# Performance work log

Hardware: AMD Instinct MI355X
Metric: run time of the kernel (lower is better)

The kernel has to match this reference:

```python
import jax, jax.numpy as jnp
import numpy as np

N_NODES = 100000
N_EDGES = 1600000
D = 128


def _gine_layer(x, src, dst, e, W1, b1, W2, b2):
    # message: relu(x_j + e_ji), aggregate: sum at destination
    m = jax.nn.relu(x[src] + e)                       # [E, D]
    agg = jax.ops.segment_sum(m, dst, num_segments=x.shape[0])  # [N, D]
    h = agg + x                                       # (1 + eps) * x_i with eps = 0
    h = jax.nn.relu(jnp.dot(h, W1) + b1)
    return jnp.dot(h, W2) + b2


def setup_inputs() -> dict:
    key = jax.random.key(0)
    ks = jax.random.split(key, 16)
    s = 0.05
    inp = {
        "x": jax.random.normal(ks[0], (N_NODES, D), dtype=jnp.float32),
        "edge_index": jax.random.randint(ks[1], (2, N_EDGES), 0, N_NODES, dtype=jnp.int64) if jax.config.jax_enable_x64 else jax.random.randint(ks[1], (2, N_EDGES), 0, N_NODES, dtype=jnp.int32),
        "edge_attr": jax.random.randint(ks[2], (N_EDGES,), 0, 100, dtype=jnp.int32),
        "edge_emb": jax.random.normal(ks[3], (100, D), dtype=jnp.float32) * s,
        "Win": jax.random.normal(ks[4], (D, D), dtype=jnp.float32) * s,
        "b_in": jnp.zeros((D,), dtype=jnp.float32),
        "W1_0": jax.random.normal(ks[5], (D, D), dtype=jnp.float32) * s,
        "b1_0": jnp.zeros((D,), dtype=jnp.float32),
        "W2_0": jax.random.normal(ks[6], (D, D), dtype=jnp.float32) * s,
        "b2_0": jnp.zeros((D,), dtype=jnp.float32),
        "W1_1": jax.random.normal(ks[7], (D, D), dtype=jnp.float32) * s,
        "b1_1": jnp.zeros((D,), dtype=jnp.float32),
        "W2_1": jax.random.normal(ks[8], (D, D), dtype=jnp.float32) * s,
        "b2_1": jnp.zeros((D,), dtype=jnp.float32),
        "Wout": jax.random.normal(ks[9], (D, 1), dtype=jnp.float32) * s,
        "b_out": jnp.zeros((1,), dtype=jnp.float32),
    }
    return inp


def reference(x, edge_index, edge_attr, edge_emb, Win, b_in,
              W1_0, b1_0, W2_0, b2_0, W1_1, b1_1, W2_1, b2_1,
              Wout, b_out):
    src, dst = edge_index[0], edge_index[1]
    e = edge_emb[edge_attr]                 # [E, D] edge-attribute embedding lookup
    h = jnp.dot(x, Win) + b_in              # input_proj
    # layer 0: GINEConv + residual add + relu (norm=none, dropout off)
    h = jax.nn.relu(_gine_layer(h, src, dst, e, W1_0, b1_0, W2_0, b2_0) + h)
    # layer 1
    h = jax.nn.relu(_gine_layer(h, src, dst, e, W1_1, b1_1, W2_1, b2_1) + h)
    # output_mlp: single Linear(hidden, 1); no final activation, no pooling
    return jnp.dot(h, Wout) + b_out
```

## Files before the change

### kernel.cpp

```cpp
#include <hip/hip_runtime.h>

#define NN 100000
#define D 128
#define CHUNK 4096
#define BCSTRIDE 392
#define AGG_BLOCKS 1024

typedef __attribute__((ext_vector_type(8))) short short8;
typedef __attribute__((ext_vector_type(8))) unsigned short ushort8;
typedef __attribute__((ext_vector_type(4))) float f32x4;

__device__ __forceinline__ float4 ld4(const float* p) { return *(const float4*)p; }

__device__ __forceinline__ unsigned short f2bf(float f) {
    unsigned int u = __float_as_uint(f);
    unsigned int r = u + 0x7fffu + ((u >> 16) & 1u);
    return (unsigned short)(r >> 16);
}
__device__ __forceinline__ float bf2f(unsigned short h) {
    return __uint_as_float(((unsigned int)h) << 16);
}
__device__ __forceinline__ int swz(int r, int c) {
    return r * 128 + ((((c >> 2) ^ (r & 7)) << 2) | (c & 3));
}

__device__ __forceinline__ void coop_gemm(
    const unsigned int* uT,
    const unsigned short* __restrict__ Whi, const unsigned short* __restrict__ Wlo,
    int wv, int L, int lr, int q, f32x4 acc[4][2])
{
    #pragma unroll
    for (int ks = 0; ks < 4; ++ks) {
        short8 ahi[4], alo[4];
        #pragma unroll
        for (int m = 0; m < 4; ++m) {
            const int row = m * 16 + lr;
            const int cb  = ks * 32 + q * 8;
            const uint4 a0 = *(const uint4*)&uT[swz(row, cb)];
            const uint4 a1 = *(const uint4*)&uT[swz(row, cb + 4)];
            const unsigned int w[8] = {a0.x, a0.y, a0.z, a0.w, a1.x, a1.y, a1.z, a1.w};
            #pragma unroll
            for (int j = 0; j < 8; ++j) {
                ahi[m][j] = (short)(w[j] >> 16);
                alo[m][j] = (short)(w[j] & 0xffffu);
            }
        }
        #pragma unroll
        for (int n = 0; n < 2; ++n) {
            const int nt = wv * 2 + n;
            const int base = ((nt * 4 + ks) * 64 + L) * 8;
            const short8 bhi = *(const short8*)&Whi[base];
            const short8 blo = *(const short8*)&Wlo[base];
            #pragma unroll
            for (int m = 0; m < 4; ++m) {
                acc[m][n] = __builtin_amdgcn_mfma_f32_16x16x32_bf16(alo[m], bhi, acc[m][n], 0, 0, 0);
                acc[m][n] = __builtin_amdgcn_mfma_f32_16x16x32_bf16(ahi[m], blo, acc[m][n], 0, 0, 0);
                acc[m][n] = __builtin_amdgcn_mfma_f32_16x16x32_bf16(ahi[m], bhi, acc[m][n], 0, 0, 0);
            }
        }
    }
}

__global__ __launch_bounds__(256) void setup_all(
    const float* __restrict__ W0, const float* __restrict__ W1,
    const float* __restrict__ W2, const float* __restrict__ W3,
    const float* __restrict__ W4, unsigned short* __restrict__ wp,
    const float* __restrict__ emb, unsigned int* __restrict__ embp,
    int* __restrict__ binTotal)
{
    const int T = blockIdx.x * 256 + threadIdx.x;
    if (T < 5 * D * D) {
        const int w = T / (D * D);
        const int t = T % (D * D);
        const float* W = (w == 0) ? W0 : (w == 1) ? W1 : (w == 2) ? W2 : (w == 3) ? W3 : W4;
        const int j  = t & 7;
        const int L  = (t >> 3) & 63;
        const int ks = (t >> 9) & 3;
        const int nt = t >> 11;
        const float v = W[(ks * 32 + (L >> 4) * 8 + j) * D + nt * 16 + (L & 15)];
        const unsigned short h = f2bf(v);
        unsigned short* hi = wp + (size_t)w * 2 * D * D;
        hi[t] = h;
        hi[D * D + t] = f2bf(v - bf2f(h));
    } else if (T < 5 * D * D + 6400) {
        const int i = T - 5 * D * D;
        embp[i] = (unsigned int)f2bf(emb[i * 2]) | ((unsigned int)f2bf(emb[i * 2 + 1]) << 16);
    } else if (T < 5 * D * D + 6400 + BCSTRIDE) {
        binTotal[T - 5 * D * D - 6400] = 0;
    }
}

__global__ __launch_bounds__(256) void gemm_in(
    const float* __restrict__ A1,
    const unsigned short* __restrict__ Whi, const unsigned short* __restrict__ Wlo,
    const float* __restrict__ bias,
    unsigned short* __restrict__ out_hi, unsigned short* __restrict__ out_lo, int N)
{
    __shared__ __align__(16) unsigned int uT[64 * 128];
    const int t  = threadIdx.x;
    const int wv = t >> 6;
    const int L  = t & 63;
    const int lr = L & 15;
    const int q  = L >> 4;
    const int rbase = wv * 16;
    const int row = blockIdx.x * 64 + rbase + lr;
    const int rl  = rbase + lr;

    #pragma unroll
    for (int ks = 0; ks < 4; ++ks) {
        float v[8];
        if (row < N) {
            const int off = row * D + ks * 32 + q * 8;
            const float4 x0 = ld4(&A1[off]), x1 = ld4(&A1[off + 4]);
            v[0] = x0.x; v[1] = x0.y; v[2] = x0.z; v[3] = x0.w;
            v[4] = x1.x; v[5] = x1.y; v[6] = x1.z; v[7] = x1.w;
        } else {
            #pragma unroll
            for (int j = 0; j < 8; ++j) v[j] = 0.f;
        }
        unsigned int pk[8];
        #pragma unroll
        for (int j = 0; j < 8; ++j) {
            const unsigned int hi = f2bf(v[j]);
            pk[j] = (hi << 16) | f2bf(v[j] - bf2f((unsigned short)hi));
        }
        const int cb = ks * 32 + q * 8;
        *(uint4*)&uT[swz(rl, cb)]     = make_uint4(pk[0], pk[1], pk[2], pk[3]);
        *(uint4*)&uT[swz(rl, cb + 4)] = make_uint4(pk[4], pk[5], pk[6], pk[7]);
    }
    __syncthreads();

    f32x4 acc[4][2];
    #pragma unroll
    for (int m = 0; m < 4; ++m)
        #pragma unroll
        for (int n = 0; n < 2; ++n) acc[m][n] = (f32x4){0.f, 0.f, 0.f, 0.f};
    coop_gemm(uT, Whi, Wlo, wv, L, lr, q, acc);
    __syncthreads();

    #pragma unroll
    for (int n = 0; n < 2; ++n) {
        const int nt = wv * 2 + n;
        const float b = bias[nt * 16 + lr];
        #pragma unroll
        for (int m = 0; m < 4; ++m)
            #pragma unroll
            for (int r = 0; r < 4; ++r)
                uT[swz(m * 16 + q * 4 + r, nt * 16 + lr)] = __float_as_uint(acc[m][n][r] + b);
    }
    __syncthreads();

    if (row < N) {
        #pragma unroll
        for (int ks = 0; ks < 4; ++ks) {
            const int cb = ks * 32 + q * 8;
            const uint4 a0 = *(const uint4*)&uT[swz(rl, cb)];
            const uint4 a1 = *(const uint4*)&uT[swz(rl, cb + 4)];
            const unsigned int w[8] = {a0.x, a0.y, a0.z, a0.w, a1.x, a1.y, a1.z, a1.w};
            const int off = row * D + cb;
            ushort8 oh, ol;
            #pragma unroll
            for (int j = 0; j < 8; ++j) {
                const float o = __uint_as_float(w[j]);
                const unsigned short h = f2bf(o);
                oh[j] = h;
                ol[j] = f2bf(o - bf2f(h));
            }
            *(ushort8*)&out_hi[off] = oh;
            *(ushort8*)&out_lo[off] = ol;
        }
    }
}

template<bool LAST>
__global__ __launch_bounds__(256) void mlp_fused(
    const float* __restrict__ agg,
    const unsigned short* h_hi, const unsigned short* h_lo,
    const unsigned short* __restrict__ W1hi, const unsigned short* __restrict__ W1lo,
    const float* __restrict__ b1,
    const unsigned short* __restrict__ W2hi, const unsigned short* __restrict__ W2lo,
    const float* __restrict__ b2,
    unsigned short* out_hi, unsigned short* out_lo,
    const float* __restrict__ Wout, const float* __restrict__ bout,
    float* __restrict__ outv, int N)
{
    __shared__ __align__(16) unsigned int uT[64 * 128];
    const int t  = threadIdx.x;
    const int wv = t >> 6;
    const int L  = t & 63;
    const int lr = L & 15;
    const int q  = L >> 4;
    const int rbase = wv * 16;
    const int row = blockIdx.x * 64 + rbase + lr;
    const int rl  = rbase + lr;

    #pragma unroll
    for (int ks = 0; ks < 4; ++ks) {
        float v[8];
        if (row < N) {
            const int off = row * D + ks * 32 + q * 8;
            const float4 x0 = ld4(&agg[off]), x1 = ld4(&agg[off + 4]);
            const ushort8 hh = *(const ushort8*)&h_hi[off];
            const ushort8 ll = *(const ushort8*)&h_lo[off];
            v[0] = x0.x; v[1] = x0.y; v[2] = x0.z; v[3] = x0.w;
            v[4] = x1.x; v[5] = x1.y; v[6] = x1.z; v[7] = x1.w;
            #pragma unroll
            for (int j = 0; j < 8; ++j) v[j] += bf2f(hh[j]) + bf2f(ll[j]);
        } else {
            #pragma unroll
            for (int j = 0; j < 8; ++j) v[j] = 0.f;
        }
        unsigned int pk[8];
        #pragma unroll
        for (int j = 0; j < 8; ++j) {
            const unsigned int hi = f2bf(v[j]);
            pk[j] = (hi << 16) | f2bf(v[j] - bf2f((unsigned short)hi));
        }
        const int cb = ks * 32 + q * 8;
        *(uint4*)&uT[swz(rl, cb)]     = make_uint4(pk[0], pk[1], pk[2], pk[3]);
        *(uint4*)&uT[swz(rl, cb + 4)] = make_uint4(pk[4], pk[5], pk[6], pk[7]);
    }
    __syncthreads();

    f32x4 acc[4][2];
    #pragma unroll
    for (int m = 0; m < 4; ++m)
        #pragma unroll
        for (int n = 0; n < 2; ++n) acc[m][n] = (f32x4){0.f, 0.f, 0.f, 0.f};
    coop_gemm(uT, W1hi, W1lo, wv, L, lr, q, acc);
    __syncthreads();

    #pragma unroll
    for (int n = 0; n < 2; ++n) {
        const int nt = wv * 2 + n;
        const float b = b1[nt * 16 + lr];
        #pragma unroll
        for (int m = 0; m < 4; ++m)
            #pragma unroll
            for (int r = 0; r < 4; ++r) {
                const float o = fmaxf(acc[m][n][r] + b, 0.f);
                const unsigned int hi = f2bf(o);
                const unsigned int lo = f2bf(o - bf2f((unsigned short)hi));
                uT[swz(m * 16 + q * 4 + r, nt * 16 + lr)] = (hi << 16) | lo;
            }
    }
    __syncthreads();

    f32x4 acc2[4][2];
    #pragma unroll
    for (int m = 0; m < 4; ++m)
        #pragma unroll
        for (int n = 0; n < 2; ++n) acc2[m][n] = (f32x4){0.f, 0.f, 0.f, 0.f};
    coop_gemm(uT, W2hi, W2lo, wv, L, lr, q, acc2);
    __syncthreads();

    #pragma unroll
    for (int n = 0; n < 2; ++n) {
        const int nt = wv * 2 + n;
        const float b = b2[nt * 16 + lr];
        #pragma unroll
        for (int m = 0; m < 4; ++m)
            #pragma unroll
            for (int r = 0; r < 4; ++r)
                uT[swz(m * 16 + q * 4 + r, nt * 16 + lr)] = __float_as_uint(acc2[m][n][r] + b);
    }
    __syncthreads();

    if (LAST) {
        float accv = 0.f;
        if (row < N) {
            #pragma unroll
            for (int ks = 0; ks < 4; ++ks) {
                const int cb = ks * 32 + q * 8;
                const uint4 a0 = *(const uint4*)&uT[swz(rl, cb)];
                const uint4 a1 = *(const uint4*)&uT[swz(rl, cb + 4)];
                const unsigned int w[8] = {a0.x, a0.y, a0.z, a0.w, a1.x, a1.y, a1.z, a1.w};
                const int off = row * D + cb;
                const ushort8 hh = *(const ushort8*)&h_hi[off];
                const ushort8 ll = *(const ushort8*)&h_lo[off];
                const float4 w0 = ld4(&Wout[cb]);
                const float4 w1 = ld4(&Wout[cb + 4]);
                float o[8];
                #pragma unroll
                for (int j = 0; j < 8; ++j)
                    o[j] = fmaxf(__uint_as_float(w[j]) + bf2f(hh[j]) + bf2f(ll[j]), 0.f);
                accv += o[0] * w0.x + o[1] * w0.y + o[2] * w0.z + o[3] * w0.w;
                accv += o[4] * w1.x + o[5] * w1.y + o[6] * w1.z + o[7] * w1.w;
            }
        }
        accv += __shfl_xor(accv, 16);
        accv += __shfl_xor(accv, 32);
        if (q == 0 && row < N) outv[row] = accv + bout[0];
    } else if (row < N) {
        #pragma unroll
        for (int ks = 0; ks < 4; ++ks) {
            const int cb = ks * 32 + q * 8;
            const uint4 a0 = *(const uint4*)&uT[swz(rl, cb)];
            const uint4 a1 = *(const uint4*)&uT[swz(rl, cb + 4)];
            const unsigned int w[8] = {a0.x, a0.y, a0.z, a0.w, a1.x, a1.y, a1.z, a1.w};
            const int off = row * D + cb;
            const ushort8 hh = *(const ushort8*)&h_hi[off];
            const ushort8 ll = *(const ushort8*)&h_lo[off];
            ushort8 oh, ol;
            #pragma unroll
            for (int j = 0; j < 8; ++j) {
                const float o = fmaxf(__uint_as_float(w[j]) + bf2f(hh[j]) + bf2f(ll[j]), 0.f);
                const unsigned short h = f2bf(o);
                oh[j] = h;
                ol[j] = f2bf(o - bf2f(h));
            }
            *(ushort8*)&out_hi[off] = oh;
            *(ushort8*)&out_lo[off] = ol;
        }
    }
}

__global__ __launch_bounds__(256) void bin_count(
    const int* __restrict__ dst, int* __restrict__ blkcnt,
    int* __restrict__ binTotal, int E, int nbins)
{
    __shared__ int hist[512];
    const int t = threadIdx.x;
    const int i = blockIdx.x;
    for (int k = t; k < nbins; k += 256) hist[k] = 0;
    __syncthreads();
    const int e0 = i * CHUNK;
    const int e1 = min(E, e0 + CHUNK);
    for (int e = e0 + t; e < e1; e += 256) atomicAdd(&hist[dst[e] >> 8], 1);
    __syncthreads();
    for (int k = t; k < nbins; k += 256) {
        const int c = hist[k];
        blkcnt[i * BCSTRIDE + k] = c;
        if (c) atomicAdd(&binTotal[k], c);
    }
}

__global__ __launch_bounds__(512) void bin_scan(
    const int* __restrict__ binTotal, int* __restrict__ binStart,
    int* __restrict__ binCursor, int nbins)
{
    __shared__ int s[512];
    const int t = threadIdx.x;
    const int v = (t < nbins) ? binTotal[t] : 0;
    s[t] = v;
    __syncthreads();
    for (int off = 1; off < 512; off <<= 1) {
        const int x = (t >= off) ? s[t - off] : 0;
        __syncthreads();
        s[t] += x;
        __syncthreads();
    }
    if (t < nbins) { binStart[t] = s[t] - v; binCursor[t] = s[t] - v; }
    if (t == 0)    binStart[nbins] = s[511];
}

__global__ __launch_bounds__(256) void bin_scatter(
    const int* __restrict__ src, const int* __restrict__ dst,
    const int* __restrict__ attr, const int* __restrict__ blkcnt,
    int* __restrict__ binCursor, int2* __restrict__ binned, int E, int nbins)
{
    __shared__ int cur[512];
    const int t = threadIdx.x;
    const int i = blockIdx.x;
    for (int k = t; k < nbins; k += 256) {
        const int c = blkcnt[i * BCSTRIDE + k];
        if (c) cur[k] = atomicAdd(&binCursor[k], c);
    }
    __syncthreads();
    const int e0 = i * CHUNK;
    const int e1 = min(E, e0 + CHUNK);
    for (int e = e0 + t; e < e1; e += 256) {
        const int d = dst[e];
        const int p = atomicAdd(&cur[d >> 8], 1);
        binned[p] = make_int2(src[e] | (attr[e] << 20), d);
    }
}

__global__ __launch_bounds__(256) void bin_build(
    const int2* __restrict__ binned, const int* __restrict__ binStart,
    int* __restrict__ rowptr, int* __restrict__ epack, int N)
{
    __shared__ int hist[256];
    __shared__ int scn[256];
    __shared__ int curn[256];
    const int t = threadIdx.x;
    const int b = blockIdx.x;
    hist[t] = 0;
    __syncthreads();
    const int ebeg = binStart[b];
    const int eend = binStart[b + 1];
    for (int e = ebeg + t; e < eend; e += 256) atomicAdd(&hist[binned[e].y & 255], 1);
    __syncthreads();
    scn[t] = hist[t];
    __syncthreads();
    for (int off = 1; off < 256; off <<= 1) {
        const int x = (t >= off) ? scn[t - off] : 0;
        __syncthreads();
        scn[t] += x;
        __syncthreads();
    }
    const int node = b * 256 + t;
    if (node < N) rowptr[node] = ebeg + scn[t];
    curn[t] = ebeg + scn[t] - hist[t];
    __syncthreads();
    for (int e = ebeg + t; e < eend; e += 256) {
        const int2 v = binned[e];
        const int p = atomicAdd(&curn[v.y & 255], 1);
        epack[p] = v.x;
    }
}

__global__ __launch_bounds__(512) void aggregate(
    const unsigned int* __restrict__ hu,
    const int* __restrict__ rowptr, const int* __restrict__ epack,
    const unsigned int* __restrict__ embp, float* __restrict__ agg, int N)
{
    __shared__ unsigned int semb[100 * 64];
    const int t = threadIdx.x;
    for (int i = t; i < 100 * 64; i += 512) semb[i] = embp[i];
    __syncthreads();

    const int wv   = t >> 6;
    const int lane = t & 63;

    for (int node = blockIdx.x * 8 + wv; node < N; node += AGG_BLOCKS * 8) {
        int start = (node == 0) ? 0 : rowptr[node - 1];
        int end   = rowptr[node];
        start = __builtin_amdgcn_readfirstlane(start);
        end   = __builtin_amdgcn_readfirstlane(end);

        float ax = 0.f, ay = 0.f;
        int j = start;

        for (; j < end && (j & 3); ++j) {
            const int p0 = __builtin_amdgcn_readfirstlane(epack[j]);
            const unsigned int u0 = hu[(p0 & 0xFFFFF) * 64 + lane];
            const unsigned int v0 = semb[(p0 >> 20) * 64 + lane];
            ax += fmaxf(__uint_as_float(u0 << 16) + __uint_as_float(v0 << 16), 0.f);
            ay += fmaxf(__uint_as_float(u0 & 0xffff0000u) + __uint_as_float(v0 & 0xffff0000u), 0.f);
        }

        for (; j + 7 < end; j += 8) {
            const int4 pk0 = *(const int4*)&epack[j];
            const int4 pk1 = *(const int4*)&epack[j + 4];
            int p[8];
            p[0] = __builtin_amdgcn_readfirstlane(pk0.x);
            p[1] = __builtin_amdgcn_readfirstlane(pk0.y);
            p[2] = __builtin_amdgcn_readfirstlane(pk0.z);
            p[3] = __builtin_amdgcn_readfirstlane(pk0.w);
            p[4] = __builtin_amdgcn_readfirstlane(pk1.x);
            p[5] = __builtin_amdgcn_readfirstlane(pk1.y);
            p[6] = __builtin_amdgcn_readfirstlane(pk1.z);
            p[7] = __builtin_amdgcn_readfirstlane(pk1.w);
            unsigned int u[8], v[8];
            #pragma unroll
            for (int k = 0; k < 8; ++k) u[k] = hu[(p[k] & 0xFFFFF) * 64 + lane];
            #pragma unroll
            for (int k = 0; k < 8; ++k) v[k] = semb[(p[k] >> 20) * 64 + lane];
            #pragma unroll
            for (int k = 0; k < 8; ++k) {
                ax += fmaxf(__uint_as_float(u[k] << 16) + __uint_as_float(v[k] << 16), 0.f);
                ay += fmaxf(__uint_as_float(u[k] & 0xffff0000u) + __uint_as_float(v[k] & 0xffff0000u), 0.f);
            }
        }

        if (j + 3 < end) {
            const int4 pk0 = *(const int4*)&epack[j];
            int p[4];
            p[0] = __builtin_amdgcn_readfirstlane(pk0.x);
            p[1] = __builtin_amdgcn_readfirstlane(pk0.y);
            p[2] = __builtin_amdgcn_readfirstlane(pk0.z);
            p[3] = __builtin_amdgcn_readfirstlane(pk0.w);
            unsigned int u[4], v[4];
            #pragma unroll
            for (int k = 0; k < 4; ++k) u[k] = hu[(p[k] & 0xFFFFF) * 64 + lane];
            #pragma unroll
            for (int k = 0; k < 4; ++k) v[k] = semb[(p[k] >> 20) * 64 + lane];
            #pragma unroll
            for (int k = 0; k < 4; ++k) {
                ax += fmaxf(__uint_as_float(u[k] << 16) + __uint_as_float(v[k] << 16), 0.f);
                ay += fmaxf(__uint_as_float(u[k] & 0xffff0000u) + __uint_as_float(v[k] & 0xffff0000u), 0.f);
            }
            j += 4;
        }

        for (; j < end; ++j) {
            const int p0 = __builtin_amdgcn_readfirstlane(epack[j]);
            const unsigned int u0 = hu[(p0 & 0xFFFFF) * 64 + lane];
            const unsigned int v0 = semb[(p0 >> 20) * 64 + lane];
            ax += fmaxf(__uint_as_float(u0 << 16) + __uint_as_float(v0 << 16), 0.f);
            ay += fmaxf(__uint_as_float(u0 & 0xffff0000u) + __uint_as_float(v0 & 0xffff0000u), 0.f);
        }

        float2 o; o.x = ax; o.y = ay;
        ((float2*)agg)[node * 64 + lane] = o;
    }
}

extern "C" void kernel_launch(void* const* d_in, const int* in_sizes, int n_in,
                              void* d_out, int out_size, void* d_ws, size_t ws_size,
                              hipStream_t stream)
{
    const float* x     = (const float*)d_in[0];
    const int*   ei    = (const int*)  d_in[1];
    const int*   attr  = (const int*)  d_in[2];
    const float* emb   = (const float*)d_in[3];
    const float* Win   = (const float*)d_in[4];
    const float* b_in  = (const float*)d_in[5];
    const float* W1_0  = (const float*)d_in[6];
    const float* b1_0  = (const float*)d_in[7];
    const float* W2_0  = (const float*)d_in[8];
    const float* b2_0  = (const float*)d_in[9];
    const float* W1_1  = (const float*)d_in[10];
    const float* b1_1  = (const float*)d_in[11];
    const float* W2_1  = (const float*)d_in[12];
    const float* b2_1  = (const float*)d_in[13];
    const float* Wout  = (const float*)d_in[14];
    const float* b_out = (const float*)d_in[15];
    float* out = (float*)d_out;

    const int N = NN;
    const int E = in_sizes[2];
    const int* srcp = ei;
    const int* dstp = ei + E;
    const int nbins = (N + 255) >> 8;
    const int eblocks = (E + CHUNK - 1) / CHUNK;

    unsigned short* h_hi = (unsigned short*)d_ws;
    unsigned short* h_lo = h_hi + (size_t)N * D;
    float* agg    = (float*)(h_lo + (size_t)N * D);
    int*   rowptr = (int*)(agg + (size_t)N * D);
    int*   epack  = rowptr + N;
    unsigned short* wp = (unsigned short*)(epack + E);
    unsigned short* Whi[5], *Wlo[5];
    for (int i = 0; i < 5; ++i) {
        Whi[i] = wp + (size_t)i * 2 * D * D;
        Wlo[i] = Whi[i] + D * D;
    }
    unsigned int* embp = (unsigned int*)(wp + 5 * 2 * D * D);
    int2* binned    = (int2*)agg;
    int*  blkcnt    = (int*)(binned + E);
    int*  binTotal  = blkcnt + eblocks * BCSTRIDE;
    int*  binStart  = binTotal + BCSTRIDE;
    int*  binCursor = binStart + BCSTRIDE;

    dim3 blk(256);
    const int fgrid = (N + 63) / 64;
    const int sgrid = (5 * D * D + 6400 + BCSTRIDE + 255) / 256;

    setup_all<<<sgrid, blk, 0, stream>>>(Win, W1_0, W2_0, W1_1, W2_1, wp, emb, embp, binTotal);

    bin_count<<<eblocks, blk, 0, stream>>>(dstp, blkcnt, binTotal, E, nbins);
    bin_scan<<<1, 512, 0, stream>>>(binTotal, binStart, binCursor, nbins);
    bin_scatter<<<eblocks, blk, 0, stream>>>(srcp, dstp, attr, blkcnt, binCursor, binned, E, nbins);
    bin_build<<<nbins, blk, 0, stream>>>(binned, binStart, rowptr, epack, N);

    gemm_in<<<fgrid, blk, 0, stream>>>(x, Whi[0], Wlo[0], b_in, h_hi, h_lo, N);

    aggregate<<<AGG_BLOCKS, dim3(512), 0, stream>>>(
        (const unsigned int*)h_hi, rowptr, epack, embp, agg, N);
    mlp_fused<false><<<fgrid, blk, 0, stream>>>(
        agg, h_hi, h_lo, Whi[1], Wlo[1], b1_0, Whi[2], Wlo[2], b2_0,
        h_hi, h_lo, nullptr, nullptr, nullptr, N);

    aggregate<<<AGG_BLOCKS, dim3(512), 0, stream>>>(
        (const unsigned int*)h_hi, rowptr, epack, embp, agg, N);
    mlp_fused<true><<<fgrid, blk, 0, stream>>>(
        agg, h_hi, h_lo, Whi[3], Wlo[3], b1_1, Whi[4], Wlo[4], b2_1,
        nullptr, nullptr, Wout, b_out, out, N);
}
```

Baseline: 440.1 us.

## Split input projection GEMM across CSR build kernels to overlap with binning

The standalone input-projection GEMM kernel is removed. Its 64-row tiles are spread across the three CSR-construction kernels (count, scatter, build) as extra blocks that run alongside the binning blocks. This is meant to fill idle compute units during the latency-bound, atomic-heavy binning phases and to remove one kernel launch. In exchange, each kernel carries the larger shared-memory footprint, and the fixed split of 200/700/rest tiles may leave the load unbalanced.

```diff
diff --git a/kernel.cpp b/kernel.cpp
--- a/kernel.cpp
+++ b/kernel.cpp
@@ -57,6 +57,88 @@
                 acc[m][n] = __builtin_amdgcn_mfma_f32_16x16x32_bf16(ahi[m], blo, acc[m][n], 0, 0, 0);
                 acc[m][n] = __builtin_amdgcn_mfma_f32_16x16x32_bf16(ahi[m], bhi, acc[m][n], 0, 0, 0);
             }
+        }
+    }
+}
+
+__device__ __forceinline__ void gemm_in_body(
+    unsigned int* uT, int bid,
+    const float* __restrict__ A1,
+    const unsigned short* __restrict__ Whi, const unsigned short* __restrict__ Wlo,
+    const float* __restrict__ bias,
+    unsigned short* __restrict__ out_hi, unsigned short* __restrict__ out_lo, int N)
+{
+    const int t  = threadIdx.x;
+    const int wv = t >> 6;
+    const int L  = t & 63;
+    const int lr = L & 15;
+    const int q  = L >> 4;
+    const int rbase = wv * 16;
+    const int row = bid * 64 + rbase + lr;
+    const int rl  = rbase + lr;
+
+    #pragma unroll
+    for (int ks = 0; ks < 4; ++ks) {
+        float v[8];
+        if (row < N) {
+            const int off = row * D + ks * 32 + q * 8;
+            const float4 x0 = ld4(&A1[off]), x1 = ld4(&A1[off + 4]);
+            v[0] = x0.x; v[1] = x0.y; v[2] = x0.z; v[3] = x0.w;
+            v[4] = x1.x; v[5] = x1.y; v[6] = x1.z; v[7] = x1.w;
+        } else {
+            #pragma unroll
+            for (int j = 0; j < 8; ++j) v[j] = 0.f;
+        }
+        unsigned int pk[8];
+        #pragma unroll
+        for (int j = 0; j < 8; ++j) {
+            const unsigned int hi = f2bf(v[j]);
+            pk[j] = (hi << 16) | f2bf(v[j] - bf2f((unsigned short)hi));
+        }
+        const int cb = ks * 32 + q * 8;
+        *(uint4*)&uT[swz(rl, cb)]     = make_uint4(pk[0], pk[1], pk[2], pk[3]);
+        *(uint4*)&uT[swz(rl, cb + 4)] = make_uint4(pk[4], pk[5], pk[6], pk[7]);
+    }
+    __syncthreads();
+
+    f32x4 acc[4][2];
+    #pragma unroll
+    for (int m = 0; m < 4; ++m)
+        #pragma unroll
+        for (int n = 0; n < 2; ++n) acc[m][n] = (f32x4){0.f, 0.f, 0.f, 0.f};
+    coop_gemm(uT, Whi, Wlo, wv, L, lr, q, acc);
+    __syncthreads();
+
+    #pragma unroll
+    for (int n = 0; n < 2; ++n) {
+        const int nt = wv * 2 + n;
+        const float b = bias[nt * 16 + lr];
+        #pragma unroll
+        for (int m = 0; m < 4; ++m)
+            #pragma unroll
+            for (int r = 0; r < 4; ++r)
+                uT[swz(m * 16 + q * 4 + r, nt * 16 + lr)] = __float_as_uint(acc[m][n][r] + b);
+    }
+    __syncthreads();
+
+    if (row < N) {
+        #pragma unroll
+        for (int ks = 0; ks < 4; ++ks) {
+            const int cb = ks * 32 + q * 8;
+            const uint4 a0 = *(const uint4*)&uT[swz(rl, cb)];
+            const uint4 a1 = *(const uint4*)&uT[swz(rl, cb + 4)];
+            const unsigned int w[8] = {a0.x, a0.y, a0.z, a0.w, a1.x, a1.y, a1.z, a1.w};
+            const int off = row * D + cb;
+            ushort8 oh, ol;
+            #pragma unroll
+            for (int j = 0; j < 8; ++j) {
+                const float o = __uint_as_float(w[j]);
+                const unsigned short h = f2bf(o);
+                oh[j] = h;
+                ol[j] = f2bf(o - bf2f(h));
+            }
+            *(ushort8*)&out_hi[off] = oh;
+            *(ushort8*)&out_lo[off] = ol;
         }
     }
 }
@@ -90,85 +172,128 @@
     }
 }
 
-__global__ __launch_bounds__(256) void gemm_in(
+__global__ __launch_bounds__(256) void fuse_count_gemm(
+    const int* __restrict__ dst, int* __restrict__ blkcnt,
+    int* __restrict__ binTotal, int E, int nbins, int csrB,
     const float* __restrict__ A1,
     const unsigned short* __restrict__ Whi, const unsigned short* __restrict__ Wlo,
     const float* __restrict__ bias,
-    unsigned short* __restrict__ out_hi, unsigned short* __restrict__ out_lo, int N)
+    unsigned short* __restrict__ out_hi, unsigned short* __restrict__ out_lo,
+    int N, int gemmBase)
 {
     __shared__ __align__(16) unsigned int uT[64 * 128];
-    const int t  = threadIdx.x;
-    const int wv = t >> 6;
-    const int L  = t & 63;
-    const int lr = L & 15;
-    const int q  = L >> 4;
-    const int rbase = wv * 16;
-    const int row = blockIdx.x * 64 + rbase + lr;
-    const int rl  = rbase + lr;
-
-    #pragma unroll
-    for (int ks = 0; ks < 4; ++ks) {
-        float v[8];
-        if (row < N) {
-            const int off = row * D + ks * 32 + q * 8;
-            const float4 x0 = ld4(&A1[off]), x1 = ld4(&A1[off + 4]);
-            v[0] = x0.x; v[1] = x0.y; v[2] = x0.z; v[3] = x0.w;
-            v[4] = x1.x; v[5] = x1.y; v[6] = x1.z; v[7] = x1.w;
-        } else {
-            #pragma unroll
-            for (int j = 0; j < 8; ++j) v[j] = 0.f;
-        }
-        unsigned int pk[8];
-        #pragma unroll
-        for (int j = 0; j < 8; ++j) {
-            const unsigned int hi = f2bf(v[j]);
-            pk[j] = (hi << 16) | f2bf(v[j] - bf2f((unsigned short)hi));
-        }
-        const int cb = ks * 32 + q * 8;
-        *(uint4*)&uT[swz(rl, cb)]     = make_uint4(pk[0], pk[1], pk[2], pk[3]);
-        *(uint4*)&uT[swz(rl, cb + 4)] = make_uint4(pk[4], pk[5], pk[6], pk[7]);
-    }
-    __syncthreads();
-
-    f32x4 acc[4][2];
-    #pragma unroll
-    for (int m = 0; m < 4; ++m)
-        #pragma unroll
-        for (int n = 0; n < 2; ++n) acc[m][n] = (f32x4){0.f, 0.f, 0.f, 0.f};
-    coop_gemm(uT, Whi, Wlo, wv, L, lr, q, acc);
-    __syncthreads();
-
-    #pragma unroll
-    for (int n = 0; n < 2; ++n) {
-        const int nt = wv * 2 + n;
-        const float b = bias[nt * 16 + lr];
-        #pragma unroll
-        for (int m = 0; m < 4; ++m)
-            #pragma unroll
-            for (int r = 0; r < 4; ++r)
-                uT[swz(m * 16 + q * 4 + r, nt * 16 + lr)] = __float_as_uint(acc[m][n][r] + b);
-    }
-    __syncthreads();
-
-    if (row < N) {
-        #pragma unroll
-        for (int ks = 0; ks < 4; ++ks) {
-            const int cb = ks * 32 + q * 8;
-            const uint4 a0 = *(const uint4*)&uT[swz(rl, cb)];
-            const uint4 a1 = *(const uint4*)&uT[swz(rl, cb + 4)];
-            const unsigned int w[8] = {a0.x, a0.y, a0.z, a0.w, a1.x, a1.y, a1.z, a1.w};
-            const int off = row * D + cb;
-            ushort8 oh, ol;
-            #pragma unroll
-            for (int j = 0; j < 8; ++j) {
-                const float o = __uint_as_float(w[j]);
-                const unsigned short h = f2bf(o);
-                oh[j] = h;
-                ol[j] = f2bf(o - bf2f(h));
-            }
-            *(ushort8*)&out_hi[off] = oh;
-            *(ushort8*)&out_lo[off] = ol;
-        }
+    if ((int)blockIdx.x < csrB) {
+        int* hist = (int*)uT;
+        const int t = threadIdx.x;
+        const int i = blockIdx.x;
+        for (int k = t; k < nbins; k += 256) hist[k] = 0;
+        __syncthreads();
+        const int e0 = i * CHUNK;
+        const int e1 = min(E, e0 + CHUNK);
+        for (int e = e0 + t; e < e1; e += 256) atomicAdd(&hist[dst[e] >> 8], 1);
+        __syncthreads();
+        for (int k = t; k < nbins; k += 256) {
+            const int c = hist[k];
+            blkcnt[i * BCSTRIDE + k] = c;
+            if (c) atomicAdd(&binTotal[k], c);
+        }
+    } else {
+        gemm_in_body(uT, blockIdx.x - csrB + gemmBase, A1, Whi, Wlo, bias, out_hi, out_lo, N);
+    }
+}
+
+__global__ __launch_bounds__(512) void bin_scan(
+    const int* __restrict__ binTotal, int* __restrict__ binStart,
+    int* __restrict__ binCursor, int nbins)
+{
+    __shared__ int s[512];
+    const int t = threadIdx.x;
+    const int v = (t < nbins) ? binTotal[t] : 0;
+    s[t] = v;
+    __syncthreads();
+    for (int off = 1; off < 512; off <<= 1) {
+        const int x = (t >= off) ? s[t - off] : 0;
+        __syncthreads();
+        s[t] += x;
+        __syncthreads();
+    }
+    if (t < nbins) { binStart[t] = s[t] - v; binCursor[t] = s[t] - v; }
+    if (t == 0)    binStart[nbins] = s[511];
+}
+
+__global__ __launch_bounds__(256) void fuse_scatter_gemm(
+    const int* __restrict__ src, const int* __restrict__ dst,
+    const int* __restrict__ attr, const int* __restrict__ blkcnt,
+    int* __restrict__ binCursor, int2* __restrict__ binned, int E, int nbins, int csrB,
+    const float* __restrict__ A1,
+    const unsigned short* __restrict__ Whi, const unsigned short* __restrict__ Wlo,
+    const float* __restrict__ bias,
+    unsigned short* __restrict__ out_hi, unsigned short* __restrict__ out_lo,
+    int N, int gemmBase)
+{
+    __shared__ __align__(16) unsigned int uT[64 * 128];
+    if ((int)blockIdx.x < csrB) {
+        int* cur = (int*)uT;
+        const int t = threadIdx.x;
+        const int i = blockIdx.x;
+        for (int k = t; k < nbins; k += 256) {
+            const int c = blkcnt[i * BCSTRIDE + k];
+            if (c) cur[k] = atomicAdd(&binCursor[k], c);
+        }
+        __syncthreads();
+        const int e0 = i * CHUNK;
+        const int e1 = min(E, e0 + CHUNK);
+        for (int e = e0 + t; e < e1; e += 256) {
+            const int d = dst[e];
+            const int p = atomicAdd(&cur[d >> 8], 1);
+            binned[p] = make_int2(src[e] | (attr[e] << 20), d);
+        }
+    } else {
+        gemm_in_body(uT, blockIdx.x - csrB + gemmBase, A1, Whi, Wlo, bias, out_hi, out_lo, N);
+    }
+}
+
+__global__ __launch_bounds__(256) void fuse_build_gemm(
+    const int2* __restrict__ binned, const int* __restrict__ binStart,
+    int* __restrict__ rowptr, int* __restrict__ epack, int csrB,
+    const float* __restrict__ A1,
+    const unsigned short* __restrict__ Whi, const unsigned short* __restrict__ Wlo,
+    const float* __restrict__ bias,
+    unsigned short* __restrict__ out_hi, unsigned short* __restrict__ out_lo,
+    int N, int gemmBase)
+{
+    __shared__ __align__(16) unsigned int uT[64 * 128];
+    if ((int)blockIdx.x < csrB) {
+        int* hist = (int*)uT;
+        int* scn  = (int*)uT + 256;
+        int* curn = (int*)uT + 512;
+        const int t = threadIdx.x;
+        const int b = blockIdx.x;
+        hist[t] = 0;
+        __syncthreads();
+        const int ebeg = binStart[b];
+        const int eend = binStart[b + 1];
+        for (int e = ebeg + t; e < eend; e += 256) atomicAdd(&hist[binned[e].y & 255], 1);
+        __syncthreads();
+        scn[t] = hist[t];
+        __syncthreads();
+        for (int off = 1; off < 256; off <<= 1) {
+            const int x = (t >= off) ? scn[t - off] : 0;
+            __syncthreads();
+            scn[t] += x;
+            __syncthreads();
+        }
+        const int node = b * 256 + t;
+        if (node < N) rowptr[node] = ebeg + scn[t];
+        curn[t] = ebeg + scn[t] - hist[t];
+        __syncthreads();
+        for (int e = ebeg + t; e < eend; e += 256) {
+            const int2 v = binned[e];
+            const int p = atomicAdd(&curn[v.y & 255], 1);
+            epack[p] = v.x;
+        }
+    } else {
+        gemm_in_body(uT, blockIdx.x - csrB + gemmBase, A1, Whi, Wlo, bias, out_hi, out_lo, N);
     }
 }
 
@@ -312,101 +437,6 @@
             *(ushort8*)&out_hi[off] = oh;
             *(ushort8*)&out_lo[off] = ol;
         }
-    }
-}
-
-__global__ __launch_bounds__(256) void bin_count(
-    const int* __restrict__ dst, int* __restrict__ blkcnt,
-    int* __restrict__ binTotal, int E, int nbins)
-{
-    __shared__ int hist[512];
-    const int t = threadIdx.x;
-    const int i = blockIdx.x;
-    for (int k = t; k < nbins; k += 256) hist[k] = 0;
-    __syncthreads();
-    const int e0 = i * CHUNK;
-    const int e1 = min(E, e0 + CHUNK);
-    for (int e = e0 + t; e < e1; e += 256) atomicAdd(&hist[dst[e] >> 8], 1);
-    __syncthreads();
-    for (int k = t; k < nbins; k += 256) {
-        const int c = hist[k];
-        blkcnt[i * BCSTRIDE + k] = c;
-        if (c) atomicAdd(&binTotal[k], c);
-    }
-}
-
-__global__ __launch_bounds__(512) void bin_scan(
-    const int* __restrict__ binTotal, int* __restrict__ binStart,
-    int* __restrict__ binCursor, int nbins)
-{
-    __shared__ int s[512];
-    const int t = threadIdx.x;
-    const int v = (t < nbins) ? binTotal[t] : 0;
-    s[t] = v;
-    __syncthreads();
-    for (int off = 1; off < 512; off <<= 1) {
-        const int x = (t >= off) ? s[t - off] : 0;
-        __syncthreads();
-        s[t] += x;
-        __syncthreads();
-    }
-    if (t < nbins) { binStart[t] = s[t] - v; binCursor[t] = s[t] - v; }
-    if (t == 0)    binStart[nbins] = s[511];
-}
-
-__global__ __launch_bounds__(256) void bin_scatter(
-    const int* __restrict__ src, const int* __restrict__ dst,
-    const int* __restrict__ attr, const int* __restrict__ blkcnt,
-    int* __restrict__ binCursor, int2* __restrict__ binned, int E, int nbins)
-{
-    __shared__ int cur[512];
-    const int t = threadIdx.x;
-    const int i = blockIdx.x;
-    for (int k = t; k < nbins; k += 256) {
-        const int c = blkcnt[i * BCSTRIDE + k];
-        if (c) cur[k] = atomicAdd(&binCursor[k], c);
-    }
-    __syncthreads();
-    const int e0 = i * CHUNK;
-    const int e1 = min(E, e0 + CHUNK);
-    for (int e = e0 + t; e < e1; e += 256) {
-        const int d = dst[e];
-        const int p = atomicAdd(&cur[d >> 8], 1);
-        binned[p] = make_int2(src[e] | (attr[e] << 20), d);
-    }
-}
-
-__global__ __launch_bounds__(256) void bin_build(
-    const int2* __restrict__ binned, const int* __restrict__ binStart,
-    int* __restrict__ rowptr, int* __restrict__ epack, int N)
-{
-    __shared__ int hist[256];
-    __shared__ int scn[256];
-    __shared__ int curn[256];
-    const int t = threadIdx.x;
-    const int b = blockIdx.x;
-    hist[t] = 0;
-    __syncthreads();
-    const int ebeg = binStart[b];
-    const int eend = binStart[b + 1];
-    for (int e = ebeg + t; e < eend; e += 256) atomicAdd(&hist[binned[e].y & 255], 1);
-    __syncthreads();
-    scn[t] = hist[t];
-    __syncthreads();
-    for (int off = 1; off < 256; off <<= 1) {
-        const int x = (t >= off) ? scn[t - off] : 0;
-        __syncthreads();
-        scn[t] += x;
-        __syncthreads();
-    }
-    const int node = b * 256 + t;
-    if (node < N) rowptr[node] = ebeg + scn[t];
-    curn[t] = ebeg + scn[t] - hist[t];
-    __syncthreads();
-    for (int e = ebeg + t; e < eend; e += 256) {
-        const int2 v = binned[e];
-        const int p = atomicAdd(&curn[v.y & 255], 1);
-        epack[p] = v.x;
     }
 }
 
@@ -548,14 +578,22 @@
     const int fgrid = (N + 63) / 64;
     const int sgrid = (5 * D * D + 6400 + BCSTRIDE + 255) / 256;
 
+    const int G1 = 200;
+    const int G2 = 700;
+    const int G3 = fgrid - G1 - G2;
+
     setup_all<<<sgrid, blk, 0, stream>>>(Win, W1_0, W2_0, W1_1, W2_1, wp, emb, embp, binTotal);
 
-    bin_count<<<eblocks, blk, 0, stream>>>(dstp, blkcnt, binTotal, E, nbins);
+    fuse_count_gemm<<<eblocks + G1, blk, 0, stream>>>(
+        dstp, blkcnt, binTotal, E, nbins, eblocks,
+        x, Whi[0], Wlo[0], b_in, h_hi, h_lo, N, 0);
     bin_scan<<<1, 512, 0, stream>>>(binTotal, binStart, binCursor, nbins);
-    bin_scatter<<<eblocks, blk, 0, stream>>>(srcp, dstp, attr, blkcnt, binCursor, binned, E, nbins);
-    bin_build<<<nbins, blk, 0, stream>>>(binned, binStart, rowptr, epack, N);
-
-    gemm_in<<<fgrid, blk, 0, stream>>>(x, Whi[0], Wlo[0], b_in, h_hi, h_lo, N);
+    fuse_scatter_gemm<<<eblocks + G2, blk, 0, stream>>>(
+        srcp, dstp, attr, blkcnt, binCursor, binned, E, nbins, eblocks,
+        x, Whi[0], Wlo[0], b_in, h_hi, h_lo, N, G1);
+    fuse_build_gemm<<<nbins + G3, blk, 0, stream>>>(
+        binned, binStart, rowptr, epack, nbins,
+        x, Whi[0], Wlo[0], b_in, h_hi, h_lo, N, G1 + G2);
 
     aggregate<<<AGG_BLOCKS, dim3(512), 0, stream>>>(
         (const unsigned int*)h_hi, rowptr, epack, embp, agg, N);
```

New measurement: 429.6 us. -2.4%, faster.
